# Performance work log

Measured on AMD Instinct MI355X. Metric: run time of the kernel, lower is better.

## Reference

```python
import jax, jax.numpy as jnp
import numpy as np

D_IN = 256
D_HID = 512

def setup_inputs() -> dict:
    key = jax.random.key(0)
    k1, k2, k3, k4, k5, k6 = jax.random.split(key, 6)
    x = jax.random.normal(k1, (8, 4096, D_IN), dtype=jnp.float32)
    adj = jax.random.uniform(k2, (8, 4096, 4096), dtype=jnp.float32)
    # GIN MLP params: Linear(256,512) -> ReLU -> Linear(512,256)
    s1 = 1.0 / np.sqrt(D_IN)
    s2 = 1.0 / np.sqrt(D_HID)
    W1 = jax.random.uniform(k3, (D_IN, D_HID), dtype=jnp.float32, minval=-s1, maxval=s1)
    b1 = jax.random.uniform(k4, (D_HID,), dtype=jnp.float32, minval=-s1, maxval=s1)
    W2 = jax.random.uniform(k5, (D_HID, D_IN), dtype=jnp.float32, minval=-s2, maxval=s2)
    b2 = jax.random.uniform(k6, (D_IN,), dtype=jnp.float32, minval=-s2, maxval=s2)
    eps = jnp.zeros((1,), dtype=jnp.float32)  # learn_eps=True, init 0
    return {"x": x, "adj": adj, "eps": eps, "W1": W1, "b1": b1, "W2": W2, "b2": b2}

def reference(x, adj, eps, W1, b1, W2, b2):
    # sum aggregation: bmm(adj, x) -> [B, N, d]
    aggregated = jnp.einsum('bnm,bmd->bnd', adj, x)
    # eps-scaled residual (learn_eps=True)
    h = (1.0 + eps) * x + aggregated
    # MLP: Linear -> ReLU -> Linear
    h = jax.nn.relu(h @ W1 + b1)
    return h @ W2 + b2
```

## Files before the change

### kernel.cpp

```cpp
#include <hip/hip_runtime.h>
#include <hip/hip_bf16.h>
#include <stdint.h>

typedef _Float16 f16;
typedef __attribute__((ext_vector_type(8))) _Float16 half8;
typedef __attribute__((ext_vector_type(4))) float f32x4;

typedef __attribute__((address_space(1))) void gvoid_t;
typedef __attribute__((address_space(3))) void lvoid_t;

__device__ __forceinline__ void dma16(const void* g, void* l) {
    __builtin_amdgcn_global_load_lds((gvoid_t*)g, (lvoid_t*)l, 16, 0, 0);
}

__global__ void __launch_bounds__(256) transpose_x_kernel(
    const float* __restrict__ x, f16* __restrict__ xT)
{
    __shared__ __align__(16) f16 tile[64][72];
    int b  = blockIdx.z;
    int m0 = blockIdx.x * 64;
    int d0 = blockIdx.y * 64;
    const float* xb = x + (size_t)b * 4096 * 256;
    f16* xTb = xT + (size_t)b * 256 * 4096;
    int tid = threadIdx.x;
    int c4 = tid & 15;
    int rb = tid >> 4;
#pragma unroll
    for (int p = 0; p < 4; ++p) {
        int row = p * 16 + rb;
        float4 v = *(const float4*)(xb + (size_t)(m0 + row) * 256 + d0 + c4 * 4);
        tile[c4 * 4 + 0][row] = (f16)v.x;
        tile[c4 * 4 + 1][row] = (f16)v.y;
        tile[c4 * 4 + 2][row] = (f16)v.z;
        tile[c4 * 4 + 3][row] = (f16)v.w;
    }
    __syncthreads();
    int mseg = tid & 7;
    int db = tid >> 3;
#pragma unroll
    for (int p = 0; p < 2; ++p) {
        int dd = p * 32 + db;
        uint4 val = *(const uint4*)&tile[dd][mseg * 8];
        *(uint4*)(xTb + (size_t)(d0 + dd) * 4096 + m0 + mseg * 8) = val;
    }
}

__global__ void __launch_bounds__(256) prep_weights_kernel(
    const float* __restrict__ W1, const float* __restrict__ W2,
    f16* __restrict__ W1T, f16* __restrict__ W2T)
{
    int idx = blockIdx.x * 256 + threadIdx.x;
    if (idx < 131072) {
        int n = idx >> 8;
        int k = idx & 255;
        W1T[idx] = (f16)W1[k * 512 + n];
    } else {
        int j = idx - 131072;
        int d = j >> 9;
        int hh = j & 511;
        W2T[j] = (f16)W2[hh * 256 + d];
    }
}

__device__ __forceinline__ void bmm_dma_tile(
    const float* adjb, const f16* xTb, float* AsBuf, f16* BsBuf,
    int kk, int wid, int lane)
{
    int a_rr = lane >> 3, a_sl = lane & 7;
#pragma unroll
    for (int c = 0; c < 2; ++c) {
        int chunk = wid + c * 8;
        int r = chunk * 8 + a_rr;
        int colg = a_sl ^ ((r & 7) ^ ((r >> 3) & 1));
        dma16(adjb + (size_t)r * 4096 + kk + colg * 4, AsBuf + chunk * 256);
    }
    int b_rr = lane >> 2, b_sl = lane & 3;
#pragma unroll
    for (int c = 0; c < 2; ++c) {
        int chunk = wid + c * 8;
        int r = chunk * 16 + b_rr;
        int colg = b_sl ^ ((r & 3) ^ ((r >> 2) & 3));
        dma16(xTb + (size_t)r * 4096 + kk + colg * 8, BsBuf + chunk * 512);
    }
}

__global__ void __launch_bounds__(512) bmm_kernel(
    const float* __restrict__ adj, const f16* __restrict__ xT,
    const float* __restrict__ x, const float* __restrict__ eps,
    f16* __restrict__ h)
{
    __shared__ __align__(16) float As[4][128 * 32];
    __shared__ __align__(16) f16  Bs[4][256 * 32];

    const int lin = blockIdx.x;
    const int b   = lin & 7;
    const int m0  = (lin >> 3) * 128;
    const int tid = threadIdx.x;
    const int lane = tid & 63, wid = tid >> 6;
    const int wm = (wid & 3) * 32;
    const int wn = (wid >> 2) * 128;
    const int l15 = lane & 15, lg = lane >> 4;

    const float* adjb = adj + (size_t)b * 4096 * 4096 + (size_t)m0 * 4096;
    const f16*   xTb  = xT  + (size_t)b * 256 * 4096;

    f32x4 acc[2][8];
#pragma unroll
    for (int i = 0; i < 2; ++i)
#pragma unroll
        for (int j = 0; j < 8; ++j) { f32x4 z = {0.f, 0.f, 0.f, 0.f}; acc[i][j] = z; }

    bmm_dma_tile(adjb, xTb, As[0], Bs[0], 0, wid, lane);
    bmm_dma_tile(adjb, xTb, As[1], Bs[1], 32, wid, lane);

    const int sA = (l15 & 7) ^ (l15 >> 3);
    const int sB = (l15 & 3) ^ ((l15 >> 2) & 3);

    for (int it = 0; it < 128; ++it) {
        if (it + 2 < 128)
            bmm_dma_tile(adjb, xTb, As[(it + 2) & 3], Bs[(it + 2) & 3],
                         (it + 2) * 32, wid, lane);

        if (it < 126)       asm volatile("s_waitcnt vmcnt(8)" ::: "memory");
        else if (it == 126) asm volatile("s_waitcnt vmcnt(4)" ::: "memory");
        else                asm volatile("s_waitcnt vmcnt(0)" ::: "memory");
        __builtin_amdgcn_s_barrier();
        asm volatile("" ::: "memory");

        const float* Ab = As[it & 3];
        const f16*  Bb  = Bs[it & 3];
        half8 af[2];
#pragma unroll
        for (int mt = 0; mt < 2; ++mt) {
            int R = wm + mt * 16 + l15;
            int p0 = (2 * lg) ^ sA;
            f32x4 a0 = *(const f32x4*)&Ab[R * 32 + p0 * 4];
            f32x4 a1 = *(const f32x4*)&Ab[R * 32 + (p0 ^ 1) * 4];
            half8 t;
            t[0] = (f16)a0.x; t[1] = (f16)a0.y; t[2] = (f16)a0.z; t[3] = (f16)a0.w;
            t[4] = (f16)a1.x; t[5] = (f16)a1.y; t[6] = (f16)a1.z; t[7] = (f16)a1.w;
            af[mt] = t;
        }
        half8 bfr[8];
        const int slotB = lg ^ sB;
#pragma unroll
        for (int nt = 0; nt < 8; ++nt) {
            int C = wn + nt * 16 + l15;
            bfr[nt] = *(const half8*)&Bb[C * 32 + slotB * 8];
        }
#pragma unroll
        for (int mt = 0; mt < 2; ++mt)
#pragma unroll
            for (int nt = 0; nt < 8; ++nt)
                acc[mt][nt] = __builtin_amdgcn_mfma_f32_16x16x32_f16(af[mt], bfr[nt], acc[mt][nt], 0, 0, 0);
    }

    float scale = 1.0f + eps[0];
    const float* xb = x + (size_t)b * 4096 * 256;
    f16* hb = h + (size_t)b * 4096 * 256;
#pragma unroll
    for (int mt = 0; mt < 2; ++mt) {
#pragma unroll
        for (int i = 0; i < 4; ++i) {
            int row = m0 + wm + mt * 16 + lg * 4 + i;
#pragma unroll
            for (int nt = 0; nt < 8; ++nt) {
                int col = wn + nt * 16 + l15;
                float hv = scale * xb[(size_t)row * 256 + col] + acc[mt][nt][i];
                hb[(size_t)row * 256 + col] = (f16)hv;
            }
        }
    }
}

__device__ __forceinline__ void mlp_dma_tile(
    const f16* Am, const f16* Bn, f16* AsBuf, f16* BsBuf,
    int kk, int K, int wid, int lane)
{
    int rr = lane >> 2, sl = lane & 3;
#pragma unroll
    for (int c = 0; c < 2; ++c) {
        int chunk = wid + c * 4;
        int r = chunk * 16 + rr;
        int colg = sl ^ ((r & 3) ^ ((r >> 2) & 3));
        dma16(Am + (size_t)r * K + kk + colg * 8, AsBuf + chunk * 512);
        dma16(Bn + (size_t)r * K + kk + colg * 8, BsBuf + chunk * 512);
    }
}

template <int K, bool RELU, bool OUTF32>
__global__ void __launch_bounds__(256) mlp_kernel(
    const f16* __restrict__ A, const f16* __restrict__ BT,
    const float* __restrict__ bias, void* __restrict__ outv, int Ntot)
{
    __shared__ __align__(16) f16 As[2][128 * 32];
    __shared__ __align__(16) f16 Bs[2][128 * 32];

    const int m0 = blockIdx.x * 128;
    const int n0 = blockIdx.y * 128;
    const int tid = threadIdx.x;
    const int lane = tid & 63, wid = tid >> 6;
    const int wm = (wid & 1) * 64;
    const int wn = (wid >> 1) * 64;
    const int l15 = lane & 15, lg = lane >> 4;

    const f16* Am = A  + (size_t)m0 * K;
    const f16* Bn = BT + (size_t)n0 * K;

    f32x4 acc[4][4];
#pragma unroll
    for (int i = 0; i < 4; ++i)
#pragma unroll
        for (int j = 0; j < 4; ++j) { f32x4 z = {0.f, 0.f, 0.f, 0.f}; acc[i][j] = z; }

    mlp_dma_tile(Am, Bn, As[0], Bs[0], 0, K, wid, lane);

    const int sf = (l15 & 3) ^ ((l15 >> 2) & 3);
    const int slot = lg ^ sf;
    const int NIT = K / 32;

    for (int it = 0; it < NIT; ++it) {
        const int buf = it & 1;
        __syncthreads();
        if (it + 1 < NIT)
            mlp_dma_tile(Am, Bn, As[buf ^ 1], Bs[buf ^ 1], (it + 1) * 32, K, wid, lane);

        half8 af[4], bf[4];
#pragma unroll
        for (int mt = 0; mt < 4; ++mt) {
            int R = wm + mt * 16 + l15;
            af[mt] = *(const half8*)&As[buf][R * 32 + slot * 8];
        }
#pragma unroll
        for (int nt = 0; nt < 4; ++nt) {
            int C = wn + nt * 16 + l15;
            bf[nt] = *(const half8*)&Bs[buf][C * 32 + slot * 8];
        }
#pragma unroll
        for (int mt = 0; mt < 4; ++mt)
#pragma unroll
            for (int nt = 0; nt < 4; ++nt)
                acc[mt][nt] = __builtin_amdgcn_mfma_f32_16x16x32_f16(af[mt], bf[nt], acc[mt][nt], 0, 0, 0);
    }

#pragma unroll
    for (int mt = 0; mt < 4; ++mt) {
#pragma unroll
        for (int i = 0; i < 4; ++i) {
            int row = m0 + wm + mt * 16 + lg * 4 + i;
#pragma unroll
            for (int nt = 0; nt < 4; ++nt) {
                int col = n0 + wn + nt * 16 + l15;
                float v = acc[mt][nt][i] + bias[col];
                if (RELU) v = v > 0.f ? v : 0.f;
                if (OUTF32)
                    ((float*)outv)[(size_t)row * Ntot + col] = v;
                else
                    ((f16*)outv)[(size_t)row * Ntot + col] = (f16)v;
            }
        }
    }
}

extern "C" void kernel_launch(void* const* d_in, const int* in_sizes, int n_in,
                              void* d_out, int out_size, void* d_ws, size_t ws_size,
                              hipStream_t stream) {
    (void)in_sizes; (void)n_in; (void)out_size; (void)ws_size;
    const float* x   = (const float*)d_in[0];
    const float* adj = (const float*)d_in[1];
    const float* eps = (const float*)d_in[2];
    const float* W1  = (const float*)d_in[3];
    const float* b1  = (const float*)d_in[4];
    const float* W2  = (const float*)d_in[5];
    const float* b2  = (const float*)d_in[6];
    float* out = (float*)d_out;

    char* ws = (char*)d_ws;
    f16* h_f16   = (f16*)(ws);
    f16* xT      = (f16*)(ws + (16u << 20));
    f16* hidden  = (f16*)(ws + (16u << 20));
    f16* W1T     = (f16*)(ws + (48u << 20));
    f16* W2T     = (f16*)(ws + (48u << 20) + 131072u * 2u * 2u);

    transpose_x_kernel<<<dim3(64, 4, 8), dim3(256), 0, stream>>>(x, xT);
    prep_weights_kernel<<<dim3(1024), dim3(256), 0, stream>>>(W1, W2, W1T, W2T);
    bmm_kernel<<<dim3(256), dim3(512), 0, stream>>>(adj, xT, x, eps, h_f16);
    mlp_kernel<256, true, false><<<dim3(256, 4), dim3(256), 0, stream>>>(h_f16, W1T, b1, (void*)hidden, 512);
    mlp_kernel<512, false, true><<<dim3(256, 2), dim3(256), 0, stream>>>(hidden, W2T, b2, (void*)out, 256);
}
```

Measured before the change: 819.9 us.

## Fuse bmm and both MLP layers into one kernel using LDS-resident h

Merges the aggregation bmm and the two MLP GEMMs into a single kernel. Each block keeps its 128x256 h tile in LDS in swizzled f16 form, computes the hidden layer in 128-wide chunks into double-buffered LDS, and accumulates the second GEMM in registers before writing the fp32 output. This removes the global round trips for h and the hidden activations and two kernel launches. In exchange, weight operands are read directly from global memory without LDS staging, and the MLP phase runs on only 256 blocks.

```diff
diff --git a/kernel.cpp b/kernel.cpp
--- a/kernel.cpp
+++ b/kernel.cpp
@@ -84,13 +84,16 @@
     }
 }
 
-__global__ void __launch_bounds__(512) bmm_kernel(
+__global__ void __launch_bounds__(512) fused_kernel(
     const float* __restrict__ adj, const f16* __restrict__ xT,
     const float* __restrict__ x, const float* __restrict__ eps,
-    f16* __restrict__ h)
+    const f16* __restrict__ W1T, const float* __restrict__ b1,
+    const f16* __restrict__ W2T, const float* __restrict__ b2,
+    float* __restrict__ out)
 {
-    __shared__ __align__(16) float As[4][128 * 32];
-    __shared__ __align__(16) f16  Bs[4][256 * 32];
+    __shared__ __align__(16) unsigned char smem[131072];
+    float* AsBase = (float*)smem;
+    f16*   BsBase = (f16*)(smem + 65536);
 
     const int lin = blockIdx.x;
     const int b   = lin & 7;
@@ -110,16 +113,18 @@
 #pragma unroll
         for (int j = 0; j < 8; ++j) { f32x4 z = {0.f, 0.f, 0.f, 0.f}; acc[i][j] = z; }
 
-    bmm_dma_tile(adjb, xTb, As[0], Bs[0], 0, wid, lane);
-    bmm_dma_tile(adjb, xTb, As[1], Bs[1], 32, wid, lane);
+    bmm_dma_tile(adjb, xTb, AsBase, BsBase, 0, wid, lane);
+    bmm_dma_tile(adjb, xTb, AsBase + 4096, BsBase + 8192, 32, wid, lane);
 
     const int sA = (l15 & 7) ^ (l15 >> 3);
     const int sB = (l15 & 3) ^ ((l15 >> 2) & 3);
 
     for (int it = 0; it < 128; ++it) {
-        if (it + 2 < 128)
-            bmm_dma_tile(adjb, xTb, As[(it + 2) & 3], Bs[(it + 2) & 3],
+        if (it + 2 < 128) {
+            int nb = (it + 2) & 3;
+            bmm_dma_tile(adjb, xTb, AsBase + nb * 4096, BsBase + nb * 8192,
                          (it + 2) * 32, wid, lane);
+        }
 
         if (it < 126)       asm volatile("s_waitcnt vmcnt(8)" ::: "memory");
         else if (it == 126) asm volatile("s_waitcnt vmcnt(4)" ::: "memory");
@@ -127,8 +132,8 @@
         __builtin_amdgcn_s_barrier();
         asm volatile("" ::: "memory");
 
-        const float* Ab = As[it & 3];
-        const f16*  Bb  = Bs[it & 3];
+        const float* Ab = AsBase + (it & 3) * 4096;
+        const f16*  Bb  = BsBase + (it & 3) * 8192;
         half8 af[2];
 #pragma unroll
         for (int mt = 0; mt < 2; ++mt) {
@@ -155,108 +160,120 @@
                 acc[mt][nt] = __builtin_amdgcn_mfma_f32_16x16x32_f16(af[mt], bfr[nt], acc[mt][nt], 0, 0, 0);
     }
 
-    float scale = 1.0f + eps[0];
-    const float* xb = x + (size_t)b * 4096 * 256;
-    f16* hb = h + (size_t)b * 4096 * 256;
-#pragma unroll
-    for (int mt = 0; mt < 2; ++mt) {
-#pragma unroll
-        for (int i = 0; i < 4; ++i) {
-            int row = m0 + wm + mt * 16 + lg * 4 + i;
+    __syncthreads();
+
+    {
+        float scale = 1.0f + eps[0];
+        const float* xb = x + (size_t)b * 4096 * 256;
+        f16* h_lds = (f16*)smem;
+#pragma unroll
+        for (int mt = 0; mt < 2; ++mt) {
+#pragma unroll
+            for (int i = 0; i < 4; ++i) {
+                int R = wm + mt * 16 + lg * 4 + i;
+                const float* xrow = xb + (size_t)(m0 + R) * 256;
+#pragma unroll
+                for (int nt = 0; nt < 8; ++nt) {
+                    int d = wn + nt * 16 + l15;
+                    float hv = scale * xrow[d] + acc[mt][nt][i];
+                    int ps = (d >> 3) ^ (R & 7);
+                    h_lds[R * 256 + ps * 8 + (d & 7)] = (f16)hv;
+                }
+            }
+        }
+    }
+    __syncthreads();
+
+#pragma unroll
+    for (int i = 0; i < 2; ++i)
+#pragma unroll
+        for (int j = 0; j < 8; ++j) { f32x4 z = {0.f, 0.f, 0.f, 0.f}; acc[i][j] = z; }
+
+    const f16* h_lds = (const f16*)smem;
+    const int wm2 = (wid & 3) * 32;
+    const int wn2 = (wid >> 2) * 64;
+
+    for (int c = 0; c < 4; ++c) {
+        f32x4 acc2[2][4];
+#pragma unroll
+        for (int i = 0; i < 2; ++i)
+#pragma unroll
+            for (int j = 0; j < 4; ++j) { f32x4 z = {0.f, 0.f, 0.f, 0.f}; acc2[i][j] = z; }
+
+#pragma unroll 2
+        for (int it2 = 0; it2 < 8; ++it2) {
+            half8 af2[2], bf2[4];
+#pragma unroll
+            for (int mt = 0; mt < 2; ++mt) {
+                int R = wm2 + mt * 16 + l15;
+                int ps = (it2 * 4 + lg) ^ (R & 7);
+                af2[mt] = *(const half8*)&h_lds[R * 256 + ps * 8];
+            }
+#pragma unroll
+            for (int nt = 0; nt < 4; ++nt) {
+                int n = c * 128 + wn2 + nt * 16 + l15;
+                bf2[nt] = *(const half8*)&W1T[(size_t)n * 256 + it2 * 32 + lg * 8];
+            }
+#pragma unroll
+            for (int mt = 0; mt < 2; ++mt)
+#pragma unroll
+                for (int nt = 0; nt < 4; ++nt)
+                    acc2[mt][nt] = __builtin_amdgcn_mfma_f32_16x16x32_f16(af2[mt], bf2[nt], acc2[mt][nt], 0, 0, 0);
+        }
+
+        f16* hid = (f16*)(smem + 65536 + (c & 1) * 32768);
+#pragma unroll
+        for (int mt = 0; mt < 2; ++mt) {
+#pragma unroll
+            for (int i = 0; i < 4; ++i) {
+                int R = wm2 + mt * 16 + lg * 4 + i;
+#pragma unroll
+                for (int nt = 0; nt < 4; ++nt) {
+                    int dc = wn2 + nt * 16 + l15;
+                    float v = acc2[mt][nt][i] + b1[c * 128 + dc];
+                    v = v > 0.f ? v : 0.f;
+                    int ps = (dc >> 3) ^ (R & 7);
+                    hid[R * 128 + ps * 8 + (dc & 7)] = (f16)v;
+                }
+            }
+        }
+        __syncthreads();
+
+        const f16* hidr = (const f16*)(smem + 65536 + (c & 1) * 32768);
+#pragma unroll
+        for (int it3 = 0; it3 < 4; ++it3) {
+            half8 af3[2], bf3[8];
+#pragma unroll
+            for (int mt = 0; mt < 2; ++mt) {
+                int R = wm + mt * 16 + l15;
+                int ps = (it3 * 4 + lg) ^ (R & 7);
+                af3[mt] = *(const half8*)&hidr[R * 128 + ps * 8];
+            }
 #pragma unroll
             for (int nt = 0; nt < 8; ++nt) {
-                int col = wn + nt * 16 + l15;
-                float hv = scale * xb[(size_t)row * 256 + col] + acc[mt][nt][i];
-                hb[(size_t)row * 256 + col] = (f16)hv;
-            }
-        }
-    }
-}
-
-__device__ __forceinline__ void mlp_dma_tile(
-    const f16* Am, const f16* Bn, f16* AsBuf, f16* BsBuf,
-    int kk, int K, int wid, int lane)
-{
-    int rr = lane >> 2, sl = lane & 3;
-#pragma unroll
-    for (int c = 0; c < 2; ++c) {
-        int chunk = wid + c * 4;
-        int r = chunk * 16 + rr;
-        int colg = sl ^ ((r & 3) ^ ((r >> 2) & 3));
-        dma16(Am + (size_t)r * K + kk + colg * 8, AsBuf + chunk * 512);
-        dma16(Bn + (size_t)r * K + kk + colg * 8, BsBuf + chunk * 512);
-    }
-}
-
-template <int K, bool RELU, bool OUTF32>
-__global__ void __launch_bounds__(256) mlp_kernel(
-    const f16* __restrict__ A, const f16* __restrict__ BT,
-    const float* __restrict__ bias, void* __restrict__ outv, int Ntot)
-{
-    __shared__ __align__(16) f16 As[2][128 * 32];
-    __shared__ __align__(16) f16 Bs[2][128 * 32];
-
-    const int m0 = blockIdx.x * 128;
-    const int n0 = blockIdx.y * 128;
-    const int tid = threadIdx.x;
-    const int lane = tid & 63, wid = tid >> 6;
-    const int wm = (wid & 1) * 64;
-    const int wn = (wid >> 1) * 64;
-    const int l15 = lane & 15, lg = lane >> 4;
-
-    const f16* Am = A  + (size_t)m0 * K;
-    const f16* Bn = BT + (size_t)n0 * K;
-
-    f32x4 acc[4][4];
-#pragma unroll
-    for (int i = 0; i < 4; ++i)
-#pragma unroll
-        for (int j = 0; j < 4; ++j) { f32x4 z = {0.f, 0.f, 0.f, 0.f}; acc[i][j] = z; }
-
-    mlp_dma_tile(Am, Bn, As[0], Bs[0], 0, K, wid, lane);
-
-    const int sf = (l15 & 3) ^ ((l15 >> 2) & 3);
-    const int slot = lg ^ sf;
-    const int NIT = K / 32;
-
-    for (int it = 0; it < NIT; ++it) {
-        const int buf = it & 1;
-        __syncthreads();
-        if (it + 1 < NIT)
-            mlp_dma_tile(Am, Bn, As[buf ^ 1], Bs[buf ^ 1], (it + 1) * 32, K, wid, lane);
-
-        half8 af[4], bf[4];
-#pragma unroll
-        for (int mt = 0; mt < 4; ++mt) {
-            int R = wm + mt * 16 + l15;
-            af[mt] = *(const half8*)&As[buf][R * 32 + slot * 8];
-        }
-#pragma unroll
-        for (int nt = 0; nt < 4; ++nt) {
-            int C = wn + nt * 16 + l15;
-            bf[nt] = *(const half8*)&Bs[buf][C * 32 + slot * 8];
-        }
-#pragma unroll
-        for (int mt = 0; mt < 4; ++mt)
-#pragma unroll
-            for (int nt = 0; nt < 4; ++nt)
-                acc[mt][nt] = __builtin_amdgcn_mfma_f32_16x16x32_f16(af[mt], bf[nt], acc[mt][nt], 0, 0, 0);
-    }
-
-#pragma unroll
-    for (int mt = 0; mt < 4; ++mt) {
-#pragma unroll
-        for (int i = 0; i < 4; ++i) {
-            int row = m0 + wm + mt * 16 + lg * 4 + i;
-#pragma unroll
-            for (int nt = 0; nt < 4; ++nt) {
-                int col = n0 + wn + nt * 16 + l15;
-                float v = acc[mt][nt][i] + bias[col];
-                if (RELU) v = v > 0.f ? v : 0.f;
-                if (OUTF32)
-                    ((float*)outv)[(size_t)row * Ntot + col] = v;
-                else
-                    ((f16*)outv)[(size_t)row * Ntot + col] = (f16)v;
+                int dcol = wn + nt * 16 + l15;
+                bf3[nt] = *(const half8*)&W2T[(size_t)dcol * 512 + c * 128 + it3 * 32 + lg * 8];
+            }
+#pragma unroll
+            for (int mt = 0; mt < 2; ++mt)
+#pragma unroll
+                for (int nt = 0; nt < 8; ++nt)
+                    acc[mt][nt] = __builtin_amdgcn_mfma_f32_16x16x32_f16(af3[mt], bf3[nt], acc[mt][nt], 0, 0, 0);
+        }
+    }
+
+    {
+        float* ob = out + ((size_t)b * 4096 + m0) * 256;
+#pragma unroll
+        for (int mt = 0; mt < 2; ++mt) {
+#pragma unroll
+            for (int i = 0; i < 4; ++i) {
+                int R = wm + mt * 16 + lg * 4 + i;
+#pragma unroll
+                for (int nt = 0; nt < 8; ++nt) {
+                    int col = wn + nt * 16 + l15;
+                    ob[(size_t)R * 256 + col] = acc[mt][nt][i] + b2[col];
+                }
             }
         }
     }
@@ -276,15 +293,12 @@
     float* out = (float*)d_out;
 
     char* ws = (char*)d_ws;
-    f16* h_f16   = (f16*)(ws);
-    f16* xT      = (f16*)(ws + (16u << 20));
-    f16* hidden  = (f16*)(ws + (16u << 20));
-    f16* W1T     = (f16*)(ws + (48u << 20));
-    f16* W2T     = (f16*)(ws + (48u << 20) + 131072u * 2u * 2u);
+    f16* xT  = (f16*)(ws);
+    f16* W1T = (f16*)(ws + (16u << 20));
+    f16* W2T = (f16*)(ws + (16u << 20) + 262144u);
 
     transpose_x_kernel<<<dim3(64, 4, 8), dim3(256), 0, stream>>>(x, xT);
     prep_weights_kernel<<<dim3(1024), dim3(256), 0, stream>>>(W1, W2, W1T, W2T);
-    bmm_kernel<<<dim3(256), dim3(512), 0, stream>>>(adj, xT, x, eps, h_f16);
-    mlp_kernel<256, true, false><<<dim3(256, 4), dim3(256), 0, stream>>>(h_f16, W1T, b1, (void*)hidden, 512);
-    mlp_kernel<512, false, true><<<dim3(256, 2), dim3(256), 0, stream>>>(hidden, W2T, b2, (void*)out, 256);
-}
+    fused_kernel<<<dim3(256), dim3(512), 0, stream>>>(adj, xT, x, eps,
+                                                      W1T, b1, W2T, b2, out);
+}
```

After: 825.6 us. About the same (+0.7%).
